# Optimization experiments

Measured on AMD Instinct MI355X. Metric: run time of the kernel, lower is better.

## Reference

```python
import jax, jax.numpy as jnp
import numpy as np


def setup_inputs() -> dict:
    key = jax.random.key(0)
    k1, k2, k3 = jax.random.split(key, 3)
    B, C, P, T = 8, 256, 16, 64
    H = 8
    d = C // H  # 32
    x = jax.random.normal(k1, (B, C, P, T), dtype=jnp.float32)
    # per-head 1x1 conv weights: project C -> d channels (Q=K=V share this conv)
    W = jax.random.normal(k2, (H, d, C), dtype=jnp.float32) * (1.0 / np.sqrt(C))
    b = jax.random.normal(k3, (H, d), dtype=jnp.float32) * 0.01
    return {"x": x, "W": W, "b": b}


def reference(x, W, b):
    B, C, P, T = x.shape
    H, d, _ = W.shape
    L = P * T
    # per-head 1x1 conv == channel contraction; Q = K = V = z
    z = jnp.einsum('bcpt,hdc->bhptd', x, W) + b[None, :, None, None, :]
    z = z.reshape(B, H, L, d)
    scale = 1.0 / jnp.sqrt(jnp.asarray(d, dtype=z.dtype))
    scores = jax.nn.softmax(jnp.einsum('bhld,bhmd->bhlm', z, z) * scale, axis=-1)
    out = jnp.einsum('bhlm,bhmd->bhld', scores, z)  # (B,H,L,d)
    # reshape back to (B, P, T, d) per head, permute to channels-first, cat heads
    out = out.reshape(B, H, P, T, d).transpose(0, 1, 4, 2, 3).reshape(B, H * d, P, T)
    return out
```

## Files before the change

kernel.cpp:

```cpp
#include <hip/hip_runtime.h>
#include <math.h>

#define BB 8
#define CC 256
#define LL 1024
#define HH 8
#define DD 32

typedef __attribute__((ext_vector_type(8))) short bf16x8;
typedef __attribute__((ext_vector_type(2))) float f32x2;
typedef __attribute__((ext_vector_type(16))) float f32x16;

#if __has_builtin(__builtin_amdgcn_exp2f)
#define EXP2F(x) __builtin_amdgcn_exp2f(x)
#else
#define EXP2F(x) exp2f(x)
#endif

__device__ inline unsigned pk2bf(float a, float b) {
  unsigned ua = __float_as_uint(a), ub = __float_as_uint(b);
  ua += 0x7FFFu + ((ua >> 16) & 1u);
  ub += 0x7FFFu + ((ub >> 16) & 1u);
  return (ua >> 16) | (ub & 0xFFFF0000u);
}

__device__ inline unsigned pk2bf_fast(float a, float b) {
  unsigned ua = __float_as_uint(a) + 0x8000u;
  unsigned ub = __float_as_uint(b) + 0x8000u;
  return __builtin_amdgcn_perm(ub, ua, 0x07060302u);
}

__global__ __launch_bounds__(256) void w16_kernel(
    const float* __restrict__ W, unsigned short* __restrict__ w16f) {
  int f = blockIdx.x * 256 + threadIdx.x;
  int lane = f & 63;
  int ks = (f >> 6) & 15;
  int head = f >> 10;
  int n = lane & 31, h = lane >> 5;
  const float* src = W + (size_t)(head * 32 + n) * CC + ks * 16 + h * 8;
  float4 a = *(const float4*)src;
  float4 c = *(const float4*)(src + 4);
  uint4 v;
  v.x = pk2bf(a.x, a.y);
  v.y = pk2bf(a.z, a.w);
  v.z = pk2bf(c.x, c.y);
  v.w = pk2bf(c.z, c.w);
  ((uint4*)w16f)[f] = v;
}

__global__ __launch_bounds__(512) void proj_mfma(
    const float* __restrict__ x, const unsigned short* __restrict__ w16f,
    const float* __restrict__ bias, unsigned short* __restrict__ z16,
    unsigned short* __restrict__ zT16) {
  __shared__ unsigned short smem[32 * 264];

  int b = blockIdx.x >> 5;
  int l0 = (blockIdx.x & 31) * 32;
  int tid = threadIdx.x;

  {
    int l = tid & 31, cg = tid >> 5;
    const float* xb = x + (size_t)b * CC * LL + l0 + l;
    unsigned short* row = &smem[l * 264 + cg * 16];
#pragma unroll
    for (int i = 0; i < 16; i += 2) {
      float f0 = xb[(size_t)(cg * 16 + i) * LL];
      float f1 = xb[(size_t)(cg * 16 + i + 1) * LL];
      *(unsigned*)&row[i] = pk2bf_fast(f0, f1);
    }
  }
  __syncthreads();

  int lane = tid & 63;
  int head = tid >> 6;
  int n = lane & 31, h = lane >> 5;

  f32x16 acc = 0.0f;
  const unsigned short* xrow = &smem[n * 264];
  const unsigned short* wf = w16f + ((size_t)head * 16) * 64 * 8;
#pragma unroll
  for (int ks = 0; ks < 16; ++ks) {
    bf16x8 bfrag = *(const bf16x8*)(xrow + ks * 16 + h * 8);
    bf16x8 afrag = *(const bf16x8*)(wf + ((size_t)ks * 64 + lane) * 8);
    acc = __builtin_amdgcn_mfma_f32_32x32x16_bf16(afrag, bfrag, acc, 0, 0, 0);
  }

  unsigned pkk[8];
  const float* bp = bias + head * DD;
#pragma unroll
  for (int g = 0; g < 4; ++g) {
    int ddb = 8 * g + 4 * h;
    float f0 = acc[4 * g + 0] + bp[ddb + 0];
    float f1 = acc[4 * g + 1] + bp[ddb + 1];
    float f2 = acc[4 * g + 2] + bp[ddb + 2];
    float f3 = acc[4 * g + 3] + bp[ddb + 3];
    unsigned p0 = pk2bf_fast(f0, f1);
    unsigned p1 = pk2bf_fast(f2, f3);
    pkk[2 * g] = p0;
    pkk[2 * g + 1] = p1;
    size_t base = (((size_t)b * HH + head) * DD + ddb) * LL + l0 + n;
    zT16[base + 0 * LL] = (unsigned short)(p0 & 0xFFFFu);
    zT16[base + 1 * LL] = (unsigned short)(p0 >> 16);
    zT16[base + 2 * LL] = (unsigned short)(p1 & 0xFFFFu);
    zT16[base + 3 * LL] = (unsigned short)(p1 >> 16);
  }

  __syncthreads();
#pragma unroll
  for (int g = 0; g < 4; ++g) {
    unsigned short* zr = &smem[n * 264 + head * 32 + 8 * g + 4 * h];
    *(unsigned*)&zr[0] = pkk[2 * g];
    *(unsigned*)&zr[2] = pkk[2 * g + 1];
  }
  __syncthreads();

  {
    int hh = tid >> 6, r = tid & 63;
    int l = r >> 1, half = r & 1;
    const unsigned short* src = &smem[l * 264 + hh * 32 + half * 16];
    uint4 v0 = *(const uint4*)src;
    uint4 v1 = *(const uint4*)(src + 8);
    unsigned short* dst =
        z16 + (((size_t)b * HH + hh) * LL + l0 + l) * DD + half * 16;
    *(uint4*)dst = v0;
    *(uint4*)(dst + 8) = v1;
  }
}

__global__ __launch_bounds__(256, 4) void attn_mfma(
    const unsigned short* __restrict__ z, const unsigned short* __restrict__ zT,
    float* __restrict__ out) {
  __shared__ float mrg[2][64][17];

  int lane = threadIdx.x & 63;
  int wave = threadIdx.x >> 6;
  int qg = wave & 1;
  int ksp = wave >> 1;
  int m = lane & 31;
  int h = lane >> 5;
  int bh = blockIdx.x >> 4;
  int qbase = (blockIdx.x & 15) * 64 + qg * 32;

  const unsigned short* zb = z + (size_t)bh * LL * DD;
  const unsigned short* zTb = zT + (size_t)bh * DD * LL;

  const float Cn2 = 0.25506441211245744f;

  bf16x8 qf0, qf1;
  {
    union { unsigned u[4]; bf16x8 v; } a, c;
    a.v = *(const bf16x8*)(zb + (size_t)(qbase + m) * DD + h * 8);
    c.v = *(const bf16x8*)(zb + (size_t)(qbase + m) * DD + 16 + h * 8);
#pragma unroll
    for (int j = 0; j < 4; ++j) {
      float lo = __uint_as_float(a.u[j] << 16) * Cn2;
      float hi = __uint_as_float(a.u[j] & 0xFFFF0000u) * Cn2;
      a.u[j] = pk2bf(lo, hi);
      float lo2 = __uint_as_float(c.u[j] << 16) * Cn2;
      float hi2 = __uint_as_float(c.u[j] & 0xFFFF0000u) * Cn2;
      c.u[j] = pk2bf(lo2, hi2);
    }
    qf0 = a.v;
    qf1 = c.v;
  }

  f32x16 O = 0.0f;
  f32x2 sum2 = {0.0f, 0.0f};
  int kstart = ksp * 512;

#define LOAD_SCORE(ti, svdst, vfd0, vfd1)                                     \
  {                                                                           \
    int kb = kstart + (ti)*32;                                                \
    bf16x8 kf0 = *(const bf16x8*)(zb + (size_t)(kb + m) * DD + h * 8);        \
    bf16x8 kf1 = *(const bf16x8*)(zb + (size_t)(kb + m) * DD + 16 + h * 8);   \
    vfd0 = *(const bf16x8*)(zTb + (size_t)m * LL + kb + h * 8);               \
    vfd1 = *(const bf16x8*)(zTb + (size_t)m * LL + kb + 16 + h * 8);          \
    svdst = 0.0f;                                                             \
    svdst = __builtin_amdgcn_mfma_f32_32x32x16_bf16(kf0, qf0, svdst, 0, 0, 0);\
    svdst = __builtin_amdgcn_mfma_f32_32x32x16_bf16(kf1, qf1, svdst, 0, 0, 0);\
  }

#define PROCESS(sv, vf0, vf1)                                                 \
  {                                                                           \
    _Pragma("unroll") for (int r = 0; r < 16; ++r) sv[r] = EXP2F(sv[r]);      \
    _Pragma("unroll") for (int r = 0; r < 16; r += 2) {                       \
      f32x2 pr = {sv[r], sv[r + 1]};                                          \
      sum2 += pr;                                                             \
    }                                                                         \
    unsigned pk[8];                                                           \
    _Pragma("unroll") for (int g = 0; g < 4; ++g) {                           \
      pk[2 * g] = pk2bf_fast(sv[4 * g], sv[4 * g + 1]);                       \
      pk[2 * g + 1] = pk2bf_fast(sv[4 * g + 2], sv[4 * g + 3]);               \
    }                                                                         \
    _Pragma("unroll") for (int h2 = 0; h2 < 2; ++h2) {                        \
      unsigned s0 = h ? pk[4 * h2] : pk[4 * h2 + 2];                          \
      unsigned s1 = h ? pk[4 * h2 + 1] : pk[4 * h2 + 3];                      \
      unsigned r0 = __shfl_xor(s0, 32, 64);                                   \
      unsigned r1 = __shfl_xor(s1, 32, 64);                                   \
      unsigned e0 = h ? r0 : pk[4 * h2];                                      \
      unsigned e1 = h ? r1 : pk[4 * h2 + 1];                                  \
      unsigned e2 = h ? pk[4 * h2 + 2] : r0;                                  \
      unsigned e3 = h ? pk[4 * h2 + 3] : r1;                                  \
      union { unsigned u[4]; bf16x8 v; } pf;                                  \
      pf.u[0] = e0; pf.u[1] = e1; pf.u[2] = e2; pf.u[3] = e3;                 \
      O = __builtin_amdgcn_mfma_f32_32x32x16_bf16(h2 ? vf1 : vf0, pf.v, O, 0, \
                                                  0, 0);                      \
    }                                                                         \
  }

  f32x16 svA, svB;
  bf16x8 vfA0, vfA1, vfB0, vfB1;

  LOAD_SCORE(0, svA, vfA0, vfA1);
#pragma unroll
  for (int i = 0; i < 8; ++i) {
    LOAD_SCORE(2 * i + 1, svB, vfB0, vfB1);
    PROCESS(svA, vfA0, vfA1);
    if (i < 7) LOAD_SCORE(2 * i + 2, svA, vfA0, vfA1);
    PROCESS(svB, vfB0, vfB1);
  }
#undef LOAD_SCORE
#undef PROCESS

  float ssum = sum2.x + sum2.y;

  if (ksp) {
#pragma unroll
    for (int r = 0; r < 16; ++r) mrg[qg][lane][r] = O[r];
    mrg[qg][lane][16] = ssum;
  }
  __syncthreads();
  if (!ksp) {
#pragma unroll
    for (int r = 0; r < 16; ++r) O[r] += mrg[qg][lane][r];
    ssum += mrg[qg][lane][16];
    ssum += __shfl_xor(ssum, 32, 64);
    float inv = 1.0f / ssum;
#pragma unroll
    for (int r = 0; r < 16; ++r) {
      int dd = (r & 3) + 8 * (r >> 2) + 4 * h;
      out[((size_t)bh * DD + dd) * LL + qbase + m] = O[r] * inv;
    }
  }
}

extern "C" void kernel_launch(void* const* d_in, const int* in_sizes, int n_in,
                              void* d_out, int out_size, void* d_ws,
                              size_t ws_size, hipStream_t stream) {
  const float* x = (const float*)d_in[0];
  const float* W = (const float*)d_in[1];
  const float* bias = (const float*)d_in[2];
  float* out = (float*)d_out;

  unsigned short* z16 = (unsigned short*)d_ws;
  unsigned short* zT16 = z16 + (size_t)BB * HH * LL * DD;
  unsigned short* w16f = zT16 + (size_t)BB * HH * LL * DD;

  hipLaunchKernelGGL(w16_kernel, dim3(32), dim3(256), 0, stream, W, w16f);
  hipLaunchKernelGGL(proj_mfma, dim3(BB * 32), dim3(512), 0, stream, x, w16f,
                     bias, z16, zT16);
  hipLaunchKernelGGL(attn_mfma, dim3(BB * HH * (LL / 64)), dim3(256), 0,
                     stream, z16, zT16, out);
}
```

Baseline: 94.67 us.

## Split projection K across waves and share K/V tiles across two query groups

The projection kernel now runs 1024 threads with two waves per head, each covering half of the channel reduction. Partial sums are merged through shared memory, and the x load and z16 store are vectorised. The attention kernel has each wave handle both 32-row query groups over a quarter of the key range, so every K/V fragment load feeds two query tiles. Partial outputs from the four waves are combined through a larger shared buffer. This halves K/V global loads per query but raises register pressure and removes the explicit software prefetch of the next tile.

```diff
diff --git a/kernel.cpp b/kernel.cpp
--- a/kernel.cpp
+++ b/kernel.cpp
@@ -48,11 +48,12 @@
   ((uint4*)w16f)[f] = v;
 }
 
-__global__ __launch_bounds__(512) void proj_mfma(
+__global__ __launch_bounds__(1024) void proj_mfma(
     const float* __restrict__ x, const unsigned short* __restrict__ w16f,
     const float* __restrict__ bias, unsigned short* __restrict__ z16,
     unsigned short* __restrict__ zT16) {
-  __shared__ unsigned short smem[32 * 264];
+  __shared__ unsigned short sm_x[32 * 264];
+  __shared__ float sm_acc[8][32][33];
 
   int b = blockIdx.x >> 5;
   int l0 = (blockIdx.x & 31) * 32;
@@ -61,126 +62,119 @@
   {
     int l = tid & 31, cg = tid >> 5;
     const float* xb = x + (size_t)b * CC * LL + l0 + l;
-    unsigned short* row = &smem[l * 264 + cg * 16];
-#pragma unroll
-    for (int i = 0; i < 16; i += 2) {
-      float f0 = xb[(size_t)(cg * 16 + i) * LL];
-      float f1 = xb[(size_t)(cg * 16 + i + 1) * LL];
-      *(unsigned*)&row[i] = pk2bf_fast(f0, f1);
-    }
-  }
-  __syncthreads();
-
-  int lane = tid & 63;
-  int head = tid >> 6;
+    unsigned p[4];
+#pragma unroll
+    for (int i = 0; i < 4; ++i) {
+      float f0 = xb[(size_t)(cg * 8 + 2 * i) * LL];
+      float f1 = xb[(size_t)(cg * 8 + 2 * i + 1) * LL];
+      p[i] = pk2bf_fast(f0, f1);
+    }
+    uint4 v = {p[0], p[1], p[2], p[3]};
+    *(uint4*)&sm_x[l * 264 + cg * 8] = v;
+  }
+  __syncthreads();
+
+  int lane = tid & 63, wave = tid >> 6;
+  int head = wave >> 1, kh = wave & 1;
   int n = lane & 31, h = lane >> 5;
 
   f32x16 acc = 0.0f;
-  const unsigned short* xrow = &smem[n * 264];
-  const unsigned short* wf = w16f + ((size_t)head * 16) * 64 * 8;
-#pragma unroll
-  for (int ks = 0; ks < 16; ++ks) {
+  const unsigned short* xrow = &sm_x[n * 264];
+  const unsigned short* wf = w16f + (size_t)(head * 16 + kh * 8) * 64 * 8;
+#pragma unroll
+  for (int s = 0; s < 8; ++s) {
+    int ks = kh * 8 + s;
     bf16x8 bfrag = *(const bf16x8*)(xrow + ks * 16 + h * 8);
-    bf16x8 afrag = *(const bf16x8*)(wf + ((size_t)ks * 64 + lane) * 8);
+    bf16x8 afrag = *(const bf16x8*)(wf + ((size_t)s * 64 + lane) * 8);
     acc = __builtin_amdgcn_mfma_f32_32x32x16_bf16(afrag, bfrag, acc, 0, 0, 0);
   }
 
-  unsigned pkk[8];
-  const float* bp = bias + head * DD;
-#pragma unroll
-  for (int g = 0; g < 4; ++g) {
-    int ddb = 8 * g + 4 * h;
-    float f0 = acc[4 * g + 0] + bp[ddb + 0];
-    float f1 = acc[4 * g + 1] + bp[ddb + 1];
-    float f2 = acc[4 * g + 2] + bp[ddb + 2];
-    float f3 = acc[4 * g + 3] + bp[ddb + 3];
-    unsigned p0 = pk2bf_fast(f0, f1);
-    unsigned p1 = pk2bf_fast(f2, f3);
-    pkk[2 * g] = p0;
-    pkk[2 * g + 1] = p1;
-    size_t base = (((size_t)b * HH + head) * DD + ddb) * LL + l0 + n;
-    zT16[base + 0 * LL] = (unsigned short)(p0 & 0xFFFFu);
-    zT16[base + 1 * LL] = (unsigned short)(p0 >> 16);
-    zT16[base + 2 * LL] = (unsigned short)(p1 & 0xFFFFu);
-    zT16[base + 3 * LL] = (unsigned short)(p1 >> 16);
-  }
-
-  __syncthreads();
-#pragma unroll
-  for (int g = 0; g < 4; ++g) {
-    unsigned short* zr = &smem[n * 264 + head * 32 + 8 * g + 4 * h];
-    *(unsigned*)&zr[0] = pkk[2 * g];
-    *(unsigned*)&zr[2] = pkk[2 * g + 1];
+  if (kh == 1) {
+#pragma unroll
+    for (int r = 0; r < 16; ++r) {
+      int row = (r & 3) + 8 * (r >> 2) + 4 * h;
+      sm_acc[head][row][n] = acc[r];
+    }
+  }
+  __syncthreads();
+
+  if (kh == 0) {
+    unsigned pkk[8];
+    const float* bp = bias + head * DD;
+#pragma unroll
+    for (int g = 0; g < 4; ++g) {
+      int ddb = 8 * g + 4 * h;
+      float f0 = acc[4 * g + 0] + sm_acc[head][ddb + 0][n] + bp[ddb + 0];
+      float f1 = acc[4 * g + 1] + sm_acc[head][ddb + 1][n] + bp[ddb + 1];
+      float f2 = acc[4 * g + 2] + sm_acc[head][ddb + 2][n] + bp[ddb + 2];
+      float f3 = acc[4 * g + 3] + sm_acc[head][ddb + 3][n] + bp[ddb + 3];
+      unsigned p0 = pk2bf_fast(f0, f1);
+      unsigned p1 = pk2bf_fast(f2, f3);
+      pkk[2 * g] = p0;
+      pkk[2 * g + 1] = p1;
+      size_t base = (((size_t)b * HH + head) * DD + ddb) * LL + l0 + n;
+      zT16[base + 0 * LL] = (unsigned short)(p0 & 0xFFFFu);
+      zT16[base + 1 * LL] = (unsigned short)(p0 >> 16);
+      zT16[base + 2 * LL] = (unsigned short)(p1 & 0xFFFFu);
+      zT16[base + 3 * LL] = (unsigned short)(p1 >> 16);
+    }
+#pragma unroll
+    for (int g = 0; g < 4; ++g) {
+      unsigned short* zr = &sm_x[n * 264 + head * 32 + 8 * g + 4 * h];
+      *(unsigned*)&zr[0] = pkk[2 * g];
+      *(unsigned*)&zr[2] = pkk[2 * g + 1];
+    }
   }
   __syncthreads();
 
   {
-    int hh = tid >> 6, r = tid & 63;
-    int l = r >> 1, half = r & 1;
-    const unsigned short* src = &smem[l * 264 + hh * 32 + half * 16];
-    uint4 v0 = *(const uint4*)src;
-    uint4 v1 = *(const uint4*)(src + 8);
-    unsigned short* dst =
-        z16 + (((size_t)b * HH + hh) * LL + l0 + l) * DD + half * 16;
-    *(uint4*)dst = v0;
-    *(uint4*)(dst + 8) = v1;
+    int l = tid >> 5, q = tid & 31;
+    uint4 v = *(const uint4*)&sm_x[l * 264 + q * 8];
+    int headl = q >> 2, dd0 = (q & 3) * 8;
+    *(uint4*)(z16 + (((size_t)b * HH + headl) * LL + l0 + l) * DD + dd0) = v;
   }
 }
 
 __global__ __launch_bounds__(256, 4) void attn_mfma(
     const unsigned short* __restrict__ z, const unsigned short* __restrict__ zT,
     float* __restrict__ out) {
-  __shared__ float mrg[2][64][17];
+  __shared__ float mrg[3][64][35];
 
   int lane = threadIdx.x & 63;
-  int wave = threadIdx.x >> 6;
-  int qg = wave & 1;
-  int ksp = wave >> 1;
+  int ksp = threadIdx.x >> 6;
   int m = lane & 31;
   int h = lane >> 5;
   int bh = blockIdx.x >> 4;
-  int qbase = (blockIdx.x & 15) * 64 + qg * 32;
+  int qbase = (blockIdx.x & 15) * 64;
 
   const unsigned short* zb = z + (size_t)bh * LL * DD;
   const unsigned short* zTb = zT + (size_t)bh * DD * LL;
-
   const float Cn2 = 0.25506441211245744f;
 
-  bf16x8 qf0, qf1;
-  {
-    union { unsigned u[4]; bf16x8 v; } a, c;
-    a.v = *(const bf16x8*)(zb + (size_t)(qbase + m) * DD + h * 8);
-    c.v = *(const bf16x8*)(zb + (size_t)(qbase + m) * DD + 16 + h * 8);
-#pragma unroll
-    for (int j = 0; j < 4; ++j) {
-      float lo = __uint_as_float(a.u[j] << 16) * Cn2;
-      float hi = __uint_as_float(a.u[j] & 0xFFFF0000u) * Cn2;
-      a.u[j] = pk2bf(lo, hi);
-      float lo2 = __uint_as_float(c.u[j] << 16) * Cn2;
-      float hi2 = __uint_as_float(c.u[j] & 0xFFFF0000u) * Cn2;
-      c.u[j] = pk2bf(lo2, hi2);
-    }
-    qf0 = a.v;
-    qf1 = c.v;
-  }
-
-  f32x16 O = 0.0f;
-  f32x2 sum2 = {0.0f, 0.0f};
-  int kstart = ksp * 512;
-
-#define LOAD_SCORE(ti, svdst, vfd0, vfd1)                                     \
-  {                                                                           \
-    int kb = kstart + (ti)*32;                                                \
-    bf16x8 kf0 = *(const bf16x8*)(zb + (size_t)(kb + m) * DD + h * 8);        \
-    bf16x8 kf1 = *(const bf16x8*)(zb + (size_t)(kb + m) * DD + 16 + h * 8);   \
-    vfd0 = *(const bf16x8*)(zTb + (size_t)m * LL + kb + h * 8);               \
-    vfd1 = *(const bf16x8*)(zTb + (size_t)m * LL + kb + 16 + h * 8);          \
-    svdst = 0.0f;                                                             \
-    svdst = __builtin_amdgcn_mfma_f32_32x32x16_bf16(kf0, qf0, svdst, 0, 0, 0);\
-    svdst = __builtin_amdgcn_mfma_f32_32x32x16_bf16(kf1, qf1, svdst, 0, 0, 0);\
-  }
-
-#define PROCESS(sv, vf0, vf1)                                                 \
+#define LOADQ(dst0, dst1, row)                                        \
+  {                                                                   \
+    union { unsigned u[4]; bf16x8 v; } a, c;                          \
+    a.v = *(const bf16x8*)(zb + (size_t)(row)*DD + h * 8);            \
+    c.v = *(const bf16x8*)(zb + (size_t)(row)*DD + 16 + h * 8);       \
+    _Pragma("unroll") for (int j = 0; j < 4; ++j) {                   \
+      a.u[j] = pk2bf(__uint_as_float(a.u[j] << 16) * Cn2,             \
+                     __uint_as_float(a.u[j] & 0xFFFF0000u) * Cn2);    \
+      c.u[j] = pk2bf(__uint_as_float(c.u[j] << 16) * Cn2,             \
+                     __uint_as_float(c.u[j] & 0xFFFF0000u) * Cn2);    \
+    }                                                                 \
+    dst0 = a.v;                                                       \
+    dst1 = c.v;                                                       \
+  }
+  bf16x8 qA0, qA1, qB0, qB1;
+  LOADQ(qA0, qA1, qbase + m);
+  LOADQ(qB0, qB1, qbase + 32 + m);
+#undef LOADQ
+
+  f32x16 OA = 0.0f, OB = 0.0f;
+  f32x2 sA = {0.0f, 0.0f}, sB = {0.0f, 0.0f};
+  int kstart = ksp * 256;
+
+#define PROCESS(sv, sum2, Odst)                                               \
   {                                                                           \
     _Pragma("unroll") for (int r = 0; r < 16; ++r) sv[r] = EXP2F(sv[r]);      \
     _Pragma("unroll") for (int r = 0; r < 16; r += 2) {                       \
@@ -203,43 +197,64 @@
       unsigned e3 = h ? pk[4 * h2 + 3] : r1;                                  \
       union { unsigned u[4]; bf16x8 v; } pf;                                  \
       pf.u[0] = e0; pf.u[1] = e1; pf.u[2] = e2; pf.u[3] = e3;                 \
-      O = __builtin_amdgcn_mfma_f32_32x32x16_bf16(h2 ? vf1 : vf0, pf.v, O, 0, \
-                                                  0, 0);                      \
+      Odst = __builtin_amdgcn_mfma_f32_32x32x16_bf16(h2 ? vf1 : vf0, pf.v,    \
+                                                     Odst, 0, 0, 0);          \
     }                                                                         \
   }
 
-  f32x16 svA, svB;
-  bf16x8 vfA0, vfA1, vfB0, vfB1;
-
-  LOAD_SCORE(0, svA, vfA0, vfA1);
-#pragma unroll
-  for (int i = 0; i < 8; ++i) {
-    LOAD_SCORE(2 * i + 1, svB, vfB0, vfB1);
-    PROCESS(svA, vfA0, vfA1);
-    if (i < 7) LOAD_SCORE(2 * i + 2, svA, vfA0, vfA1);
-    PROCESS(svB, vfB0, vfB1);
-  }
-#undef LOAD_SCORE
+#pragma unroll 2
+  for (int t = 0; t < 8; ++t) {
+    int kb = kstart + t * 32;
+    bf16x8 kf0 = *(const bf16x8*)(zb + (size_t)(kb + m) * DD + h * 8);
+    bf16x8 kf1 = *(const bf16x8*)(zb + (size_t)(kb + m) * DD + 16 + h * 8);
+    bf16x8 vf0 = *(const bf16x8*)(zTb + (size_t)m * LL + kb + h * 8);
+    bf16x8 vf1 = *(const bf16x8*)(zTb + (size_t)m * LL + kb + 16 + h * 8);
+
+    f32x16 svA = 0.0f, svB = 0.0f;
+    svA = __builtin_amdgcn_mfma_f32_32x32x16_bf16(kf0, qA0, svA, 0, 0, 0);
+    svA = __builtin_amdgcn_mfma_f32_32x32x16_bf16(kf1, qA1, svA, 0, 0, 0);
+    svB = __builtin_amdgcn_mfma_f32_32x32x16_bf16(kf0, qB0, svB, 0, 0, 0);
+    svB = __builtin_amdgcn_mfma_f32_32x32x16_bf16(kf1, qB1, svB, 0, 0, 0);
+
+    PROCESS(svA, sA, OA);
+    PROCESS(svB, sB, OB);
+  }
 #undef PROCESS
 
-  float ssum = sum2.x + sum2.y;
+  float ssA = sA.x + sA.y, ssB = sB.x + sB.y;
 
   if (ksp) {
-#pragma unroll
-    for (int r = 0; r < 16; ++r) mrg[qg][lane][r] = O[r];
-    mrg[qg][lane][16] = ssum;
-  }
-  __syncthreads();
-  if (!ksp) {
-#pragma unroll
-    for (int r = 0; r < 16; ++r) O[r] += mrg[qg][lane][r];
-    ssum += mrg[qg][lane][16];
-    ssum += __shfl_xor(ssum, 32, 64);
-    float inv = 1.0f / ssum;
+    float* d = mrg[ksp - 1][lane];
+#pragma unroll
+    for (int r = 0; r < 16; ++r) {
+      d[r] = OA[r];
+      d[16 + r] = OB[r];
+    }
+    d[32] = ssA;
+    d[33] = ssB;
+  }
+  __syncthreads();
+  if (ksp == 0) {
+#pragma unroll
+    for (int w = 0; w < 3; ++w) {
+      const float* d = mrg[w][lane];
+#pragma unroll
+      for (int r = 0; r < 16; ++r) {
+        OA[r] += d[r];
+        OB[r] += d[16 + r];
+      }
+      ssA += d[32];
+      ssB += d[33];
+    }
+    ssA += __shfl_xor(ssA, 32, 64);
+    ssB += __shfl_xor(ssB, 32, 64);
+    float invA = 1.0f / ssA, invB = 1.0f / ssB;
 #pragma unroll
     for (int r = 0; r < 16; ++r) {
       int dd = (r & 3) + 8 * (r >> 2) + 4 * h;
-      out[((size_t)bh * DD + dd) * LL + qbase + m] = O[r] * inv;
+      float* ob = out + ((size_t)bh * DD + dd) * LL + qbase;
+      ob[m] = OA[r] * invA;
+      ob[32 + m] = OB[r] * invB;
     }
   }
 }
@@ -257,7 +272,7 @@
   unsigned short* w16f = zT16 + (size_t)BB * HH * LL * DD;
 
   hipLaunchKernelGGL(w16_kernel, dim3(32), dim3(256), 0, stream, W, w16f);
-  hipLaunchKernelGGL(proj_mfma, dim3(BB * 32), dim3(512), 0, stream, x, w16f,
+  hipLaunchKernelGGL(proj_mfma, dim3(BB * 32), dim3(1024), 0, stream, x, w16f,
                      bias, z16, zT16);
   hipLaunchKernelGGL(attn_mfma, dim3(BB * HH * (LL / 64)), dim3(256), 0,
                      stream, z16, zT16, out);
```

After: 88.37 us. 6.7% less time.
